# Kernel tuning notes

Hardware: AMD Instinct MI355X
Metric: run time of the kernel (lower is better)

## Reference

```python
import jax, jax.numpy as jnp
import numpy as np

TEMPERATURE = 0.07
MASK_VAL = -65504.0  # torch code's fill value (fp16 min), note: applied BEFORE temperature division
EPS = 1e-8


def setup_inputs() -> dict:
    key = jax.random.key(0)
    z = jax.random.normal(key, (8192, 1024), dtype=jnp.float32)
    return {"z": z}


def reference(z):
    N = z.shape[0]
    # cosine similarity via normalized GEMM (torch clamps norm at eps)
    norms = jnp.maximum(jnp.linalg.norm(z, axis=-1, keepdims=True), EPS)
    zn = z / norms
    cos_sim = zn @ zn.T  # [N, N]
    eye = jnp.eye(N, dtype=bool)
    cos_sim = jnp.where(eye, MASK_VAL, cos_sim) / TEMPERATURE
    # pos_mask = eye rolled by N//2 along dim 0 -> pos_mask[i, (i - N//2) % N] = True
    idx = jnp.arange(N)
    pos = cos_sim[idx, (idx - N // 2) % N]
    nll = -pos + jax.nn.logsumexp(cos_sim, axis=-1)
    return nll.mean()
```

## Files before the change

### kernel.cpp

```cpp
#include <hip/hip_runtime.h>
#include <hip/hip_bf16.h>


#define N 8192
#define D 1024
#define INV_T 14.285714285714286f
#define NTILES 528
#define ACC_SCALE (INV_T / 1024.0f)

typedef float f32x4 __attribute__((ext_vector_type(4)));
typedef long lx2 __attribute__((ext_vector_type(2)));

#define WAITV(n) asm volatile("s_waitcnt vmcnt(" #n ")" ::: "memory")

__device__ inline void gload16(const void* g, void* l) {
  __builtin_amdgcn_global_load_lds(
      (const __attribute__((address_space(1))) void*)g,
      (__attribute__((address_space(3))) void*)l, 16, 0, 0);
}

__global__ __launch_bounds__(256) void k_normalize(const float* __restrict__ z,
                                                   unsigned char* __restrict__ zn8,
                                                   float* __restrict__ rowsum) {
  const int gt = blockIdx.x * 256 + threadIdx.x;
  if (gt < N) rowsum[gt] = 0.0f;
  const int row = gt >> 6;
  const int l = threadIdx.x & 63;
  const float4* zr = (const float4*)(z + (size_t)row * D);
  float4 v[4];
  float ss = 0.f;
#pragma unroll
  for (int j = 0; j < 4; ++j) {
    v[j] = zr[l + 64 * j];
    ss += v[j].x * v[j].x + v[j].y * v[j].y + v[j].z * v[j].z + v[j].w * v[j].w;
  }
#pragma unroll
  for (int off = 32; off > 0; off >>= 1) ss += __shfl_xor(ss, off, 64);
  const float sc = 32.0f / fmaxf(sqrtf(ss), 1e-8f);
  int* orow = (int*)(zn8 + (size_t)row * D);
#pragma unroll
  for (int j = 0; j < 4; ++j) {
    int p = __builtin_amdgcn_cvt_pk_fp8_f32(v[j].x * sc, v[j].y * sc, 0, false);
    p = __builtin_amdgcn_cvt_pk_fp8_f32(v[j].z * sc, v[j].w * sc, p, true);
    orow[l + 64 * j] = p;
  }
}

__global__ __launch_bounds__(512, 2) void k_tile(const unsigned char* __restrict__ zn8,
                                                 float* __restrict__ rowsum,
                                                 float* __restrict__ pos) {
  extern __shared__ __align__(16) char smem[];
  const int tid = threadIdx.x;
  const int w = tid >> 6, l = tid & 63;

  const int b = blockIdx.x;
  int tr = (int)((sqrtf(8.0f * (float)b + 1.0f) - 1.0f) * 0.5f);
  if (tr * (tr + 1) / 2 > b) --tr;
  if ((tr + 1) * (tr + 2) / 2 <= b) ++tr;
  const int tc = b - tr * (tr + 1) / 2;
  const bool diag = (tr == tc);

  const int wr = w >> 1, wc = w & 1;
  const int m = l & 15, kg = l >> 4;
  const int rowA0 = tr * 256, colB0 = tc * 256;

  f32x4 acc[4][8] = {};

  int srow[2], scol[2];
#pragma unroll
  for (int j = 0; j < 2; ++j) {
    int s = j * 512 + tid;
    int r = s >> 2;
    srow[j] = r;
    scol[j] = (s & 3) ^ ((r >> 1) & 3);
  }

  const int csw = (kg ^ ((m >> 1) & 3)) * 16;

#pragma unroll
  for (int p = 0; p < 2; ++p) {
    const size_t kb = (size_t)p * 64;
    char* ab = smem + p * 32768;
    char* bb = ab + 16384;
#pragma unroll
    for (int j = 0; j < 2; ++j) {
      const int s = j * 512 + tid;
      gload16((const char*)zn8 + ((size_t)(rowA0 + srow[j]) * D + kb + scol[j] * 16), ab + s * 16);
    }
    if (!diag) {
#pragma unroll
      for (int j = 0; j < 2; ++j) {
        const int s = j * 512 + tid;
        gload16((const char*)zn8 + ((size_t)(colB0 + srow[j]) * D + kb + scol[j] * 16), bb + s * 16);
      }
    }
  }

  for (int kt = 0; kt < 16; ++kt) {
    if (kt < 14) {
      const size_t kb = (size_t)(kt + 2) * 64;
      char* ab = smem + ((kt + 2) & 3) * 32768;
#pragma unroll
      for (int j = 0; j < 2; ++j) {
        const int s = j * 512 + tid;
        gload16((const char*)zn8 + ((size_t)(rowA0 + srow[j]) * D + kb + scol[j] * 16), ab + s * 16);
      }
      if (!diag) {
        char* bb = ab + 16384;
#pragma unroll
        for (int j = 0; j < 2; ++j) {
          const int s = j * 512 + tid;
          gload16((const char*)zn8 + ((size_t)(colB0 + srow[j]) * D + kb + scol[j] * 16), bb + s * 16);
        }
      }
    }
    if (!diag) {
      if (kt < 14) WAITV(8);
      else if (kt == 14) WAITV(4);
      else WAITV(0);
    } else {
      if (kt < 14) WAITV(4);
      else if (kt == 14) WAITV(2);
      else WAITV(0);
    }
    __builtin_amdgcn_s_barrier();
    asm volatile("" ::: "memory");

    const char* ab = smem + (kt & 3) * 32768;
    const char* bb = diag ? ab : (ab + 16384);

    lx2 a[4];
#pragma unroll
    for (int mt = 0; mt < 4; ++mt) {
      const char* rp = ab + (wr * 64 + mt * 16 + m) * 64;
      a[mt] = *(const lx2*)(rp + csw);
    }
#pragma unroll
    for (int nt = 0; nt < 8; ++nt) {
      const char* rp = bb + (wc * 128 + nt * 16 + m) * 64;
      const lx2 bfrag = *(const lx2*)(rp + csw);
#pragma unroll
      for (int mt = 0; mt < 4; ++mt) {
        acc[mt][nt] = __builtin_amdgcn_mfma_f32_16x16x32_fp8_fp8(a[mt].x, bfrag.x, acc[mt][nt], 0, 0, 0);
        acc[mt][nt] = __builtin_amdgcn_mfma_f32_16x16x32_fp8_fp8(a[mt].y, bfrag.y, acc[mt][nt], 0, 0, 0);
      }
    }
  }

  const int quad = l >> 4;
  const int col = l & 15;
  float cs[8] = {0.f, 0.f, 0.f, 0.f, 0.f, 0.f, 0.f, 0.f};
#pragma unroll
  for (int mt = 0; mt < 4; ++mt) {
    float rs[4] = {0.f, 0.f, 0.f, 0.f};
#pragma unroll
    for (int nt = 0; nt < 8; ++nt) {
      const int gcol = colB0 + wc * 128 + nt * 16 + col;
#pragma unroll
      for (int r = 0; r < 4; ++r) {
        const int grow = rowA0 + wr * 64 + mt * 16 + quad * 4 + r;
        const float t = acc[mt][nt][r] * ACC_SCALE;
        if (gcol == (grow ^ (N / 2))) {
          pos[grow] = t;
          pos[gcol] = t;
        }
        const float e = (gcol == grow) ? 0.0f : __expf(t - INV_T);
        rs[r] += e;
        cs[nt] += e;
      }
    }
#pragma unroll
    for (int off = 1; off < 16; off <<= 1) {
#pragma unroll
      for (int r = 0; r < 4; ++r) rs[r] += __shfl_xor(rs[r], off, 64);
    }
    if (col == 0) {
#pragma unroll
      for (int r = 0; r < 4; ++r)
        atomicAdd(&rowsum[rowA0 + wr * 64 + mt * 16 + quad * 4 + r], rs[r]);
    }
  }
  if (!diag) {
#pragma unroll
    for (int nt = 0; nt < 8; ++nt) {
      cs[nt] += __shfl_xor(cs[nt], 16, 64);
      cs[nt] += __shfl_xor(cs[nt], 32, 64);
    }
    if (l < 16) {
#pragma unroll
      for (int nt = 0; nt < 8; ++nt)
        atomicAdd(&rowsum[colB0 + wc * 128 + nt * 16 + l], cs[nt]);
    }
  }
}

__global__ __launch_bounds__(1024) void k_final(const float* __restrict__ rowsum,
                                                const float* __restrict__ pos,
                                                float* __restrict__ out) {
  const int t = threadIdx.x;
  float s = 0.f;
  for (int i = t; i < N; i += 1024) s += INV_T + __logf(rowsum[i]) - pos[i];
#pragma unroll
  for (int off = 32; off > 0; off >>= 1) s += __shfl_down(s, off, 64);
  __shared__ float red[16];
  if ((t & 63) == 0) red[t >> 6] = s;
  __syncthreads();
  if (t == 0) {
    float tot = 0.f;
#pragma unroll
    for (int j = 0; j < 16; ++j) tot += red[j];
    out[0] = tot * (1.0f / N);
  }
}

extern "C" void kernel_launch(void* const* d_in, const int* in_sizes, int n_in,
                              void* d_out, int out_size, void* d_ws, size_t ws_size,
                              hipStream_t stream) {
  const float* z = (const float*)d_in[0];
  float* out = (float*)d_out;
  char* ws = (char*)d_ws;
  unsigned char* zn8 = (unsigned char*)ws;
  float* rowsum = (float*)(ws + (size_t)N * D);
  float* pos = (float*)(ws + (size_t)N * D + (size_t)N * 4);

  static bool attr_set = false;
  if (!attr_set) {
    hipFuncSetAttribute((const void*)k_tile,
                        hipFuncAttributeMaxDynamicSharedMemorySize, 131072);
    attr_set = true;
  }

  k_normalize<<<N / 4, 256, 0, stream>>>(z, zn8, rowsum);
  k_tile<<<NTILES, 512, 131072, stream>>>(zn8, rowsum, pos);
  k_final<<<1, 1024, 0, stream>>>(rowsum, pos, out);
}
```

Measured before the change: 154.7 us.

## Interleave LDS reads and MFMA phases with barriers and priority; schedule diagonal tiles last

The k-loop is restructured into four phases per k-step. Each phase loads two B fragments from LDS, waits on lgkmcnt, and runs MFMAs under raised wave priority (s_setprio), with extra barriers so the waves in a block stay in step. The prefetch of stage kt+2 is now issued after the first LDS reads, and the vmcnt wait moves to the end of each iteration. Block indexing is also changed so the 496 off-diagonal tiles get the low block IDs and the 32 cheaper diagonal tiles run last. The extra barriers per k-step add sync overhead that could offset the gain from overlapping memory and compute.

Result: slower. 158.2 us (+2.2%).

```diff
diff --git a/kernel.cpp b/kernel.cpp
--- a/kernel.cpp
+++ b/kernel.cpp
@@ -5,13 +5,19 @@
 #define N 8192
 #define D 1024
 #define INV_T 14.285714285714286f
-#define NTILES 528
+#define NOFF 496
+#define NBLK 528
 #define ACC_SCALE (INV_T / 1024.0f)
 
 typedef float f32x4 __attribute__((ext_vector_type(4)));
 typedef long lx2 __attribute__((ext_vector_type(2)));
 
 #define WAITV(n) asm volatile("s_waitcnt vmcnt(" #n ")" ::: "memory")
+#define LGKM0                                      \
+  do {                                             \
+    asm volatile("s_waitcnt lgkmcnt(0)" ::: "memory"); \
+    __builtin_amdgcn_sched_barrier(0);             \
+  } while (0)
 
 __device__ inline void gload16(const void* g, void* l) {
   __builtin_amdgcn_global_load_lds(
@@ -42,7 +48,7 @@
   for (int j = 0; j < 4; ++j) {
     int p = __builtin_amdgcn_cvt_pk_fp8_f32(v[j].x * sc, v[j].y * sc, 0, false);
     p = __builtin_amdgcn_cvt_pk_fp8_f32(v[j].z * sc, v[j].w * sc, p, true);
-    orow[l + 64 * j] = p;
+    orow[j * 64 + l] = p;
   }
 }
 
@@ -52,103 +58,111 @@
   extern __shared__ __align__(16) char smem[];
   const int tid = threadIdx.x;
   const int w = tid >> 6, l = tid & 63;
-
-  const int b = blockIdx.x;
-  int tr = (int)((sqrtf(8.0f * (float)b + 1.0f) - 1.0f) * 0.5f);
-  if (tr * (tr + 1) / 2 > b) --tr;
-  if ((tr + 1) * (tr + 2) / 2 <= b) ++tr;
-  const int tc = b - tr * (tr + 1) / 2;
-  const bool diag = (tr == tc);
-
   const int wr = w >> 1, wc = w & 1;
   const int m = l & 15, kg = l >> 4;
+  const int quad = l >> 4, col = l & 15;
+
+  const int b = blockIdx.x;
+  int tr, tc;
+  if (b < NOFF) {
+    const int q = b;
+    tr = (int)((1.0f + sqrtf(8.0f * (float)q + 1.0f)) * 0.5f);
+    if (tr * (tr - 1) / 2 > q) --tr;
+    if (tr * (tr + 1) / 2 <= q) ++tr;
+    tc = q - tr * (tr - 1) / 2;
+  } else {
+    tr = tc = b - NOFF;
+  }
+  const bool diag = (tr == tc);
   const int rowA0 = tr * 256, colB0 = tc * 256;
 
-  f32x4 acc[4][8] = {};
-
   int srow[2], scol[2];
 #pragma unroll
   for (int j = 0; j < 2; ++j) {
-    int s = j * 512 + tid;
-    int r = s >> 2;
+    const int s = j * 512 + tid;
+    const int r = s >> 2;
     srow[j] = r;
     scol[j] = (s & 3) ^ ((r >> 1) & 3);
   }
-
   const int csw = (kg ^ ((m >> 1) & 3)) * 16;
 
-#pragma unroll
-  for (int p = 0; p < 2; ++p) {
-    const size_t kb = (size_t)p * 64;
-    char* ab = smem + p * 32768;
-    char* bb = ab + 16384;
+  f32x4 acc[4][8] = {};
+
+  auto stage = [&](int kt2) {
+    const size_t kb = (size_t)kt2 * 64;
+    char* ab = smem + (kt2 & 3) * 32768;
 #pragma unroll
     for (int j = 0; j < 2; ++j) {
       const int s = j * 512 + tid;
       gload16((const char*)zn8 + ((size_t)(rowA0 + srow[j]) * D + kb + scol[j] * 16), ab + s * 16);
     }
     if (!diag) {
+      char* bb = ab + 16384;
 #pragma unroll
       for (int j = 0; j < 2; ++j) {
         const int s = j * 512 + tid;
         gload16((const char*)zn8 + ((size_t)(colB0 + srow[j]) * D + kb + scol[j] * 16), bb + s * 16);
       }
     }
-  }
+  };
+
+  stage(0);
+  stage(1);
+  if (!diag) WAITV(4); else WAITV(2);
+  __syncthreads();
 
   for (int kt = 0; kt < 16; ++kt) {
-    if (kt < 14) {
-      const size_t kb = (size_t)(kt + 2) * 64;
-      char* ab = smem + ((kt + 2) & 3) * 32768;
-#pragma unroll
-      for (int j = 0; j < 2; ++j) {
-        const int s = j * 512 + tid;
-        gload16((const char*)zn8 + ((size_t)(rowA0 + srow[j]) * D + kb + scol[j] * 16), ab + s * 16);
-      }
-      if (!diag) {
-        char* bb = ab + 16384;
-#pragma unroll
-        for (int j = 0; j < 2; ++j) {
-          const int s = j * 512 + tid;
-          gload16((const char*)zn8 + ((size_t)(colB0 + srow[j]) * D + kb + scol[j] * 16), bb + s * 16);
-        }
-      }
-    }
-    if (!diag) {
-      if (kt < 14) WAITV(8);
-      else if (kt == 14) WAITV(4);
-      else WAITV(0);
-    } else {
-      if (kt < 14) WAITV(4);
-      else if (kt == 14) WAITV(2);
-      else WAITV(0);
-    }
-    __builtin_amdgcn_s_barrier();
-    asm volatile("" ::: "memory");
-
     const char* ab = smem + (kt & 3) * 32768;
     const char* bb = diag ? ab : (ab + 16384);
 
     lx2 a[4];
 #pragma unroll
+    for (int mt = 0; mt < 4; ++mt)
+      a[mt] = *(const lx2*)(ab + (wr * 64 + mt * 16 + m) * 64 + csw);
+    lx2 b0 = *(const lx2*)(bb + (wc * 128 + 0 * 16 + m) * 64 + csw);
+    lx2 b1 = *(const lx2*)(bb + (wc * 128 + 1 * 16 + m) * 64 + csw);
+    if (kt < 14) stage(kt + 2);
+    __builtin_amdgcn_s_barrier();
+    LGKM0;
+    __builtin_amdgcn_s_setprio(1);
+#pragma unroll
     for (int mt = 0; mt < 4; ++mt) {
-      const char* rp = ab + (wr * 64 + mt * 16 + m) * 64;
-      a[mt] = *(const lx2*)(rp + csw);
-    }
-#pragma unroll
-    for (int nt = 0; nt < 8; ++nt) {
-      const char* rp = bb + (wc * 128 + nt * 16 + m) * 64;
-      const lx2 bfrag = *(const lx2*)(rp + csw);
+      acc[mt][0] = __builtin_amdgcn_mfma_f32_16x16x32_fp8_fp8(a[mt].x, b0.x, acc[mt][0], 0, 0, 0);
+      acc[mt][0] = __builtin_amdgcn_mfma_f32_16x16x32_fp8_fp8(a[mt].y, b0.y, acc[mt][0], 0, 0, 0);
+      acc[mt][1] = __builtin_amdgcn_mfma_f32_16x16x32_fp8_fp8(a[mt].x, b1.x, acc[mt][1], 0, 0, 0);
+      acc[mt][1] = __builtin_amdgcn_mfma_f32_16x16x32_fp8_fp8(a[mt].y, b1.y, acc[mt][1], 0, 0, 0);
+    }
+    __builtin_amdgcn_s_setprio(0);
+    __builtin_amdgcn_s_barrier();
+
+#pragma unroll
+    for (int ph = 1; ph < 4; ++ph) {
+      const int n0 = 2 * ph;
+      b0 = *(const lx2*)(bb + (wc * 128 + n0 * 16 + m) * 64 + csw);
+      b1 = *(const lx2*)(bb + (wc * 128 + (n0 + 1) * 16 + m) * 64 + csw);
+      __builtin_amdgcn_s_barrier();
+      LGKM0;
+      __builtin_amdgcn_s_setprio(1);
 #pragma unroll
       for (int mt = 0; mt < 4; ++mt) {
-        acc[mt][nt] = __builtin_amdgcn_mfma_f32_16x16x32_fp8_fp8(a[mt].x, bfrag.x, acc[mt][nt], 0, 0, 0);
-        acc[mt][nt] = __builtin_amdgcn_mfma_f32_16x16x32_fp8_fp8(a[mt].y, bfrag.y, acc[mt][nt], 0, 0, 0);
+        acc[mt][n0] = __builtin_amdgcn_mfma_f32_16x16x32_fp8_fp8(a[mt].x, b0.x, acc[mt][n0], 0, 0, 0);
+        acc[mt][n0] = __builtin_amdgcn_mfma_f32_16x16x32_fp8_fp8(a[mt].y, b0.y, acc[mt][n0], 0, 0, 0);
+        acc[mt][n0 + 1] = __builtin_amdgcn_mfma_f32_16x16x32_fp8_fp8(a[mt].x, b1.x, acc[mt][n0 + 1], 0, 0, 0);
+        acc[mt][n0 + 1] = __builtin_amdgcn_mfma_f32_16x16x32_fp8_fp8(a[mt].y, b1.y, acc[mt][n0 + 1], 0, 0, 0);
       }
-    }
-  }
-
-  const int quad = l >> 4;
-  const int col = l & 15;
+      __builtin_amdgcn_s_setprio(0);
+      if (ph < 3) __builtin_amdgcn_s_barrier();
+    }
+
+    if (kt < 14) {
+      if (!diag) WAITV(4); else WAITV(2);
+    } else if (kt == 14) {
+      WAITV(0);
+    }
+    __builtin_amdgcn_s_barrier();
+  }
+  asm volatile("" ::: "memory");
+
   float cs[8] = {0.f, 0.f, 0.f, 0.f, 0.f, 0.f, 0.f, 0.f};
 #pragma unroll
   for (int mt = 0; mt < 4; ++mt) {
@@ -231,6 +245,6 @@
   }
 
   k_normalize<<<N / 4, 256, 0, stream>>>(z, zn8, rowsum);
-  k_tile<<<NTILES, 512, 131072, stream>>>(zn8, rowsum, pos);
+  k_tile<<<NBLK, 512, 131072, stream>>>(zn8, rowsum, pos);
   k_final<<<1, 1024, 0, stream>>>(rowsum, pos, out);
 }
```
